# Performance work log

Measured on AMD Instinct MI355X. Metric: run time of the kernel, lower is better.

The kernel has to match this reference:

```python
import jax, jax.numpy as jnp
import numpy as np


def _dct2(x):
    """DCT-II over last dim, scipy norm=None scaling (matches the torch rfft trick:
    X_k = 2 * sum_n x_n cos(pi*k*(2n+1)/(2N))). Expressed as one batched matmul."""
    N = x.shape[-1]
    n = jnp.arange(N, dtype=x.dtype)
    k = jnp.arange(N, dtype=x.dtype)
    # D[k, n] = 2*cos(pi*k*(2n+1)/(2N))
    D = 2.0 * jnp.cos((np.pi / (2.0 * N)) * k[:, None] * (2.0 * n[None, :] + 1.0))
    return jnp.einsum('kn,bcn->bck', D, x)


def setup_inputs() -> dict:
    key = jax.random.key(0)
    k0, k1, k2 = jax.random.split(key, 3)
    b, c, l = 32, 512, 1024
    x = jax.random.normal(k0, (b, c, l), dtype=jnp.float32)
    # 1x1 Conv1d weights (kernel_size=1, bias=False) stored as [out, in]
    w1 = jax.random.normal(k1, (2 * c, c), dtype=jnp.float32) / np.float32(np.sqrt(c))
    w2 = jax.random.normal(k2, (c, 2 * c), dtype=jnp.float32) / np.float32(np.sqrt(2 * c))
    ln_w = jnp.ones((l,), dtype=jnp.float32)
    ln_b = jnp.zeros((l,), dtype=jnp.float32)
    return {"x": x, "w1": w1, "w2": w2, "ln_w": ln_w, "ln_b": ln_b}


def reference(x, w1, w2, ln_w, ln_b):
    eps = 1e-6
    freq = _dct2(x)                                   # [b, c, l]
    mu = jnp.mean(freq, axis=-1, keepdims=True)
    var = jnp.var(freq, axis=-1, keepdims=True)       # biased, like nn.LayerNorm
    h = (freq - mu) * jax.lax.rsqrt(var + eps) * ln_w + ln_b
    # fc: Conv1d(c->2c, k=1) -> Dropout(eval: identity) -> ReLU -> Conv1d(2c->c) -> Sigmoid
    h = jax.nn.relu(jnp.einsum('oi,bil->bol', w1, h))  # [b, 2c, l]
    gate = jax.nn.sigmoid(jnp.einsum('oi,bil->bol', w2, h))  # [b, c, l]
    return x * gate
```

## Files before the change

### kernel.cpp

```cpp
#include <hip/hip_runtime.h>
#include <hip/hip_bf16.h>
#include <math.h>

typedef short short8 __attribute__((ext_vector_type(8)));
typedef short short4v __attribute__((ext_vector_type(4)));
typedef float f32x4 __attribute__((ext_vector_type(4)));

__device__ __forceinline__ short f2bf(float f) {
  union { float f; unsigned u; } v; v.f = f;
  unsigned r = v.u + 0x7FFFu + ((v.u >> 16) & 1u);
  return (short)(r >> 16);
}
__device__ __forceinline__ float bf2f(short s) {
  union { unsigned u; float f; } v; v.u = ((unsigned)(unsigned short)s) << 16;
  return v.f;
}

__global__ __launch_bounds__(256) void cast_kernel(const float* __restrict__ in,
                                                   short* __restrict__ out, int n4) {
  int i = blockIdx.x * blockDim.x + threadIdx.x;
  if (i < n4) {
    float4 v = ((const float4*)in)[i];
    short4v o;
    o.x = f2bf(v.x); o.y = f2bf(v.y); o.z = f2bf(v.z); o.w = f2bf(v.w);
    ((short4v*)out)[i] = o;
  }
}

__global__ __launch_bounds__(256) void prep_eo(const float* __restrict__ x,
                                               short* __restrict__ eo) {
  int t = blockIdx.x * 256 + threadIdx.x;
  int bc = t >> 7, n0 = (t & 127) * 4;
  const float* xr = x + (size_t)bc * 1024;
  float4 f = *(const float4*)(xr + n0);
  float4 r = *(const float4*)(xr + 1020 - n0);
  short4v ef, of;
  ef.x = f2bf(f.x + r.w); ef.y = f2bf(f.y + r.z); ef.z = f2bf(f.z + r.y); ef.w = f2bf(f.w + r.x);
  of.x = f2bf(f.x - r.w); of.y = f2bf(f.y - r.z); of.z = f2bf(f.z - r.y); of.w = f2bf(f.w - r.x);
  *(short4v*)&eo[(size_t)bc * 512 + n0] = ef;
  *(short4v*)&eo[8388608 + (size_t)bc * 512 + n0] = of;
}

__global__ __launch_bounds__(256) void build_Deo(short* __restrict__ D) {
  int t = blockIdx.x * 256 + threadIdx.x;
  int parity = t >> 18, rem = t & 262143;
  int k2 = rem >> 9, n = rem & 511;
  const float s = 1.5339807878856412e-03f;
  float arg = (s * (float)(2 * k2 + parity)) * (float)(2 * n + 1);
  D[t] = f2bf(2.0f * cosf(arg));
}

__global__ __launch_bounds__(256) void ln_stats(const float2* __restrict__ partial,
                                                float2* __restrict__ musd) {
  int n = blockIdx.x * 256 + threadIdx.x;
  float S = 0.f, Q = 0.f;
#pragma unroll
  for (int r = 0; r < 16; ++r) {
    float2 p = partial[(size_t)r * 16384 + n];
    S += p.x; Q += p.y;
  }
  float mu  = S * (1.f / 1024.f);
  float var = Q * (1.f / 1024.f) - mu * mu;
  float2 o; o.x = mu; o.y = rsqrtf(var + 1e-6f);
  musd[n] = o;
}

__global__ __launch_bounds__(256) void ln_apply(short* __restrict__ freqT,
                                                const float2* __restrict__ musd,
                                                const float* __restrict__ lnw,
                                                const float* __restrict__ lnb) {
  int t = blockIdx.x * 256 + threadIdx.x;
  int c8 = t & 63;
  int k  = (t >> 6) & 1023;
  int b  = t >> 16;
  size_t idx = ((size_t)b << 19) + (size_t)k * 512 + (size_t)c8 * 8;
  short8 v = *(const short8*)&freqT[idx];
  float w  = lnw[k];
  float bb = lnb[k];
  const float2* ms = &musd[b * 512 + c8 * 8];
  short8 o;
#pragma unroll
  for (int j = 0; j < 8; ++j) {
    float f = bf2f(v[j]);
    float2 m = ms[j];
    o[j] = f2bf((f - m.x) * m.y * w + bb);
  }
  *(short8*)&freqT[idx] = o;
}

template<int EPI, int MI>
__global__ __launch_bounds__(256, (MI == 2 ? 3 : 2)) void gemmT(
    const short* __restrict__ A, const short* __restrict__ B,
    void* __restrict__ Cout, const float* __restrict__ X,
    float2* __restrict__ P, int K, int NT, long strideA, long strideB)
{
  __shared__ short As[2][MI * 2048];
  __shared__ short Bs[2][8192];
  const int tid = threadIdx.x;
  const int l   = tid & 63;
  const int w   = tid >> 6;
  const int wm  = w >> 1;
  const int wc  = w & 1;
  const int l7  = l & 7;
  const int lr  = l & 15;
  const int lhi = l >> 4;

  const int nwg = gridDim.x, q = nwg >> 3, orig = blockIdx.x;
  const int wgid = (orig & 7) * q + (orig >> 3);
  int bx, by, bz;
  if (EPI == 0)      { bx = wgid & 7; bz = (wgid >> 3) & 1;  by = wgid >> 4; }
  else if (EPI == 1) { by = wgid & 7; bx = (wgid >> 3) & 15; bz = wgid >> 7; }
  else               { bx = wgid & 7; by = (wgid >> 3) & 7;  bz = wgid >> 6; }

  const long row0 = (long)bx * (MI * 32), col0 = (long)by * 128;
  const short* Ab = A + (size_t)bz * strideA + (size_t)row0 * K;
  const short* Bb = B + (size_t)bz * strideB + (size_t)col0 * K;

  const int rowb  = tid >> 3;
  const int slot  = tid & 7;
  const int colel = (slot ^ (rowb & 7)) * 8;
  const int abase = (wm * (MI * 16) + lr) * 64;
  const int bbase = (wc * 64 + lr) * 64;
  const int s0 = ((lhi    ) ^ l7) * 8;
  const int s1 = ((lhi + 4) ^ l7) * 8;

  f32x4 acc[MI][4];
#pragma unroll
  for (int i = 0; i < MI; ++i)
#pragma unroll
    for (int j = 0; j < 4; ++j) acc[i][j] = (f32x4){0.f, 0.f, 0.f, 0.f};

#define GLL(SRC, DST) __builtin_amdgcn_global_load_lds(                      \
      (const __attribute__((address_space(1))) void*)(SRC),                  \
      (__attribute__((address_space(3))) void*)(DST), 16, 0, 0)

#define STAGE(KT, D) do {                                                    \
    const size_t ko_ = (size_t)(KT) * 64 + colel;                            \
    _Pragma("unroll")                                                        \
    for (int r_ = 0; r_ < MI; ++r_)                                          \
      GLL(Ab + (size_t)(r_ * 32 + rowb) * K + ko_,                           \
          &As[D][(r_ * 32 + rowb) * 64 + slot * 8]);                         \
    _Pragma("unroll")                                                        \
    for (int r_ = 0; r_ < 4; ++r_)                                           \
      GLL(Bb + (size_t)(r_ * 32 + rowb) * K + ko_,                           \
          &Bs[D][(r_ * 32 + rowb) * 64 + slot * 8]);                         \
  } while (0)

#define LD8(PTR, OFF) (*(const short8*)&(PTR)[OFF])
#define MFMA(AV, BV, C) __builtin_amdgcn_mfma_f32_16x16x32_bf16(AV, BV, C, 0, 0, 0)
#define SBAR __builtin_amdgcn_s_barrier()
#define SCHB __builtin_amdgcn_sched_barrier(0)

  STAGE(0, 0);
  STAGE(1, 1);

  int cur = 0;
  for (int kt = 0; kt < NT; ++kt) {
    if (kt + 1 < NT) {
      if constexpr (MI == 2) { asm volatile("s_waitcnt vmcnt(6)" ::: "memory"); }
      else                   { asm volatile("s_waitcnt vmcnt(8)" ::: "memory"); }
    } else                   { asm volatile("s_waitcnt vmcnt(0)" ::: "memory"); }
    SCHB; SBAR;
    const short* Ad = As[cur];
    const short* Bd = Bs[cur];
    short8 af0[MI], af1[MI], bf0v[4], bf1v[4];
#pragma unroll
    for (int i = 0; i < MI; ++i) af0[i] = LD8(Ad, abase + i * 1024 + s0);
#pragma unroll
    for (int n = 0; n < 4; ++n)  bf0v[n] = LD8(Bd, bbase + n * 1024 + s0);
#pragma unroll
    for (int i = 0; i < MI; ++i) af1[i] = LD8(Ad, abase + i * 1024 + s1);
#pragma unroll
    for (int n = 0; n < 4; ++n)  bf1v[n] = LD8(Bd, bbase + n * 1024 + s1);
    SCHB;
    if constexpr (MI == 2) { asm volatile("s_waitcnt lgkmcnt(6)" ::: "memory"); }
    else                   { asm volatile("s_waitcnt lgkmcnt(8)" ::: "memory"); }
    SCHB;
    __builtin_amdgcn_s_setprio(1);
#pragma unroll
    for (int i = 0; i < MI; ++i)
#pragma unroll
      for (int n = 0; n < 4; ++n) acc[i][n] = MFMA(af0[i], bf0v[n], acc[i][n]);
    __builtin_amdgcn_s_setprio(0);
    SCHB;
    asm volatile("s_waitcnt lgkmcnt(0)" ::: "memory");
    SCHB; SBAR;
    if (kt + 2 < NT) STAGE(kt + 2, cur);
    SCHB;
    __builtin_amdgcn_s_setprio(1);
#pragma unroll
    for (int i = 0; i < MI; ++i)
#pragma unroll
      for (int n = 0; n < 4; ++n) acc[i][n] = MFMA(af1[i], bf1v[n], acc[i][n]);
    __builtin_amdgcn_s_setprio(0);
    SCHB;
    cur ^= 1;
  }

  float sv[4], qv[4];
#pragma unroll
  for (int ni = 0; ni < 4; ++ni) { sv[ni] = 0.f; qv[ni] = 0.f; }

#pragma unroll
  for (int mi = 0; mi < MI; ++mi) {
#pragma unroll
    for (int ni = 0; ni < 4; ++ni) {
#pragma unroll
      for (int j = 0; j < 4; ++j) {
        int r  = (int)row0 + wm * (MI * 16) + mi * 16 + lhi * 4 + j;
        int cc = (int)col0 + wc * 64 + ni * 16 + lr;
        float v = acc[mi][ni][j];
        if (EPI == 0) {
          sv[ni] += v; qv[ni] += v * v;
          int rr = r * 2 + bz;
          ((short*)Cout)[((size_t)(cc >> 9) << 19) + (size_t)rr * 512 + (cc & 511)] = f2bf(v);
        } else if (EPI == 1) {
          ((short*)Cout)[(size_t)bz * 1048576 + (size_t)r * 1024 + cc] = f2bf(v > 0.f ? v : 0.f);
        } else {
          size_t idx = (size_t)bz * 524288 + (size_t)r * 1024 + cc;
          float g = 1.f / (1.f + __expf(-v));
          ((float*)Cout)[idx] = X[idx] * g;
        }
      }
    }
  }

  if (EPI == 0) {
    __syncthreads();
    float* redS = (float*)&As[0][0];
    float* redQ = redS + 1024;
    const int contrib = wm * 4 + lhi;
#pragma unroll
    for (int ni = 0; ni < 4; ++ni) {
      int ccl = wc * 64 + ni * 16 + lr;
      redS[ccl * 8 + contrib] = sv[ni];
      redQ[ccl * 8 + contrib] = qv[ni];
    }
    __syncthreads();
    if (tid < 128) {
      float S = 0.f, Q = 0.f;
#pragma unroll
      for (int i = 0; i < 8; ++i) { S += redS[tid * 8 + i]; Q += redQ[tid * 8 + i]; }
      float2 o; o.x = S; o.y = Q;
      P[(size_t)(bz * 8 + bx) * 16384 + col0 + tid] = o;
    }
  }
#undef MFMA
#undef LD8
#undef STAGE
#undef GLL
#undef SBAR
#undef SCHB
}

extern "C" void kernel_launch(void* const* d_in, const int* in_sizes, int n_in,
                              void* d_out, int out_size, void* d_ws, size_t ws_size,
                              hipStream_t stream) {
  const float* x    = (const float*)d_in[0];
  const float* w1   = (const float*)d_in[1];
  const float* w2   = (const float*)d_in[2];
  const float* ln_w = (const float*)d_in[3];
  const float* ln_b = (const float*)d_in[4];
  float* out = (float*)d_out;

  char* ws = (char*)d_ws;
  short* Deo    = (short*)(ws);
  short* w1_bf  = (short*)(ws + 1048576);
  short* w2_bf  = (short*)(ws + 2097152);
  short* freqT  = (short*)(ws + 3145728);
  short* z1t    = (short*)(ws + 36700160);
  short* eo     = z1t;
  float2* part  = (float2*)(ws + 103809024);
  float2* musd  = (float2*)(ws + 105906176);

  prep_eo<<<dim3(8192), dim3(256), 0, stream>>>(x, eo);
  cast_kernel<<<dim3(512), dim3(256), 0, stream>>>(w1, w1_bf, 524288 / 4);
  cast_kernel<<<dim3(512), dim3(256), 0, stream>>>(w2, w2_bf, 524288 / 4);
  build_Deo<<<dim3(2048), dim3(256), 0, stream>>>(Deo);

  gemmT<0, 2><<<dim3(2048), dim3(256), 0, stream>>>(
      Deo, eo, (void*)freqT, nullptr, part, 512, 8, 262144, 8388608);

  ln_stats<<<dim3(64), dim3(256), 0, stream>>>(part, musd);

  ln_apply<<<dim3(8192), dim3(256), 0, stream>>>(freqT, musd, ln_w, ln_b);

  gemmT<1, 2><<<dim3(4096), dim3(256), 0, stream>>>(
      freqT, w1_bf, (void*)z1t, nullptr, nullptr, 512, 8, 524288, 0);

  gemmT<2, 2><<<dim3(2048), dim3(256), 0, stream>>>(
      w2_bf, z1t, (void*)out, x, nullptr, 1024, 16, 0, 1048576);
}
```

Baseline: 170.3 us.

## Enlarge GEMM tiles to 256x128 with a K-step of 32

```diff
diff --git a/kernel.cpp b/kernel.cpp
--- a/kernel.cpp
+++ b/kernel.cpp
@@ -55,7 +55,7 @@
   int n = blockIdx.x * 256 + threadIdx.x;
   float S = 0.f, Q = 0.f;
 #pragma unroll
-  for (int r = 0; r < 16; ++r) {
+  for (int r = 0; r < 4; ++r) {
     float2 p = partial[(size_t)r * 16384 + n];
     S += p.x; Q += p.y;
   }
@@ -88,45 +88,40 @@
   *(short8*)&freqT[idx] = o;
 }
 
-template<int EPI, int MI>
-__global__ __launch_bounds__(256, (MI == 2 ? 3 : 2)) void gemmT(
+template<int EPI>
+__global__ __launch_bounds__(256, 2) void gemmF(
     const short* __restrict__ A, const short* __restrict__ B,
     void* __restrict__ Cout, const float* __restrict__ X,
     float2* __restrict__ P, int K, int NT, long strideA, long strideB)
 {
-  __shared__ short As[2][MI * 2048];
-  __shared__ short Bs[2][8192];
+  __shared__ short As[2][8192];
+  __shared__ short Bs[2][4096];
   const int tid = threadIdx.x;
   const int l   = tid & 63;
   const int w   = tid >> 6;
   const int wm  = w >> 1;
   const int wc  = w & 1;
-  const int l7  = l & 7;
   const int lr  = l & 15;
   const int lhi = l >> 4;
 
   const int nwg = gridDim.x, q = nwg >> 3, orig = blockIdx.x;
   const int wgid = (orig & 7) * q + (orig >> 3);
   int bx, by, bz;
-  if (EPI == 0)      { bx = wgid & 7; bz = (wgid >> 3) & 1;  by = wgid >> 4; }
-  else if (EPI == 1) { by = wgid & 7; bx = (wgid >> 3) & 15; bz = wgid >> 7; }
-  else               { bx = wgid & 7; by = (wgid >> 3) & 7;  bz = wgid >> 6; }
-
-  const long row0 = (long)bx * (MI * 32), col0 = (long)by * 128;
+  if (EPI == 0)      { bx = wgid & 1; bz = (wgid >> 1) & 1; by = wgid >> 2; }
+  else if (EPI == 1) { by = wgid & 7; bx = (wgid >> 3) & 3; bz = wgid >> 5; }
+  else               { bx = wgid & 1; by = (wgid >> 1) & 7; bz = wgid >> 4; }
+
+  const long row0 = (long)bx * 256, col0 = (long)by * 128;
   const short* Ab = A + (size_t)bz * strideA + (size_t)row0 * K;
   const short* Bb = B + (size_t)bz * strideB + (size_t)col0 * K;
 
-  const int rowb  = tid >> 3;
-  const int slot  = tid & 7;
-  const int colel = (slot ^ (rowb & 7)) * 8;
-  const int abase = (wm * (MI * 16) + lr) * 64;
-  const int bbase = (wc * 64 + lr) * 64;
-  const int s0 = ((lhi    ) ^ l7) * 8;
-  const int s1 = ((lhi + 4) ^ l7) * 8;
-
-  f32x4 acc[MI][4];
-#pragma unroll
-  for (int i = 0; i < MI; ++i)
+  const int sx    = (lhi ^ ((lr >> 1) & 3)) * 8;
+  const int abase = (wm * 128 + lr) * 32;
+  const int bbase = (wc * 64  + lr) * 32;
+
+  f32x4 acc[8][4];
+#pragma unroll
+  for (int i = 0; i < 8; ++i)
 #pragma unroll
     for (int j = 0; j < 4; ++j) acc[i][j] = (f32x4){0.f, 0.f, 0.f, 0.f};
 
@@ -135,15 +130,19 @@
       (__attribute__((address_space(3))) void*)(DST), 16, 0, 0)
 
 #define STAGE(KT, D) do {                                                    \
-    const size_t ko_ = (size_t)(KT) * 64 + colel;                            \
+    const size_t kb_ = (size_t)(KT) * 32;                                    \
     _Pragma("unroll")                                                        \
-    for (int r_ = 0; r_ < MI; ++r_)                                          \
-      GLL(Ab + (size_t)(r_ * 32 + rowb) * K + ko_,                           \
-          &As[D][(r_ * 32 + rowb) * 64 + slot * 8]);                         \
+    for (int r_ = 0; r_ < 4; ++r_) {                                         \
+      int c_ = r_ * 256 + tid; int row_ = c_ >> 2; int sl_ = c_ & 3;         \
+      int sc_ = (sl_ ^ ((row_ >> 1) & 3)) * 8;                               \
+      GLL(Ab + (size_t)row_ * K + kb_ + sc_, &As[D][row_ * 32 + sl_ * 8]);   \
+    }                                                                        \
     _Pragma("unroll")                                                        \
-    for (int r_ = 0; r_ < 4; ++r_)                                           \
-      GLL(Bb + (size_t)(r_ * 32 + rowb) * K + ko_,                           \
-          &Bs[D][(r_ * 32 + rowb) * 64 + slot * 8]);                         \
+    for (int r_ = 0; r_ < 2; ++r_) {                                         \
+      int c_ = r_ * 256 + tid; int row_ = c_ >> 2; int sl_ = c_ & 3;         \
+      int sc_ = (sl_ ^ ((row_ >> 1) & 3)) * 8;                               \
+      GLL(Bb + (size_t)row_ * K + kb_ + sc_, &Bs[D][row_ * 32 + sl_ * 8]);   \
+    }                                                                        \
   } while (0)
 
 #define LD8(PTR, OFF) (*(const short8*)&(PTR)[OFF])
@@ -151,36 +150,40 @@
 #define SBAR __builtin_amdgcn_s_barrier()
 #define SCHB __builtin_amdgcn_sched_barrier(0)
 
+#define MROW(MI, AV)                                                         \
+    acc[MI][0] = MFMA(AV, b0, acc[MI][0]);                                   \
+    acc[MI][1] = MFMA(AV, b1, acc[MI][1]);                                   \
+    acc[MI][2] = MFMA(AV, b2, acc[MI][2]);                                   \
+    acc[MI][3] = MFMA(AV, b3, acc[MI][3]);
+
   STAGE(0, 0);
   STAGE(1, 1);
 
   int cur = 0;
   for (int kt = 0; kt < NT; ++kt) {
-    if (kt + 1 < NT) {
-      if constexpr (MI == 2) { asm volatile("s_waitcnt vmcnt(6)" ::: "memory"); }
-      else                   { asm volatile("s_waitcnt vmcnt(8)" ::: "memory"); }
-    } else                   { asm volatile("s_waitcnt vmcnt(0)" ::: "memory"); }
+    if (kt + 1 < NT) { asm volatile("s_waitcnt vmcnt(6)" ::: "memory"); }
+    else             { asm volatile("s_waitcnt vmcnt(0)" ::: "memory"); }
     SCHB; SBAR;
     const short* Ad = As[cur];
     const short* Bd = Bs[cur];
-    short8 af0[MI], af1[MI], bf0v[4], bf1v[4];
-#pragma unroll
-    for (int i = 0; i < MI; ++i) af0[i] = LD8(Ad, abase + i * 1024 + s0);
-#pragma unroll
-    for (int n = 0; n < 4; ++n)  bf0v[n] = LD8(Bd, bbase + n * 1024 + s0);
-#pragma unroll
-    for (int i = 0; i < MI; ++i) af1[i] = LD8(Ad, abase + i * 1024 + s1);
-#pragma unroll
-    for (int n = 0; n < 4; ++n)  bf1v[n] = LD8(Bd, bbase + n * 1024 + s1);
-    SCHB;
-    if constexpr (MI == 2) { asm volatile("s_waitcnt lgkmcnt(6)" ::: "memory"); }
-    else                   { asm volatile("s_waitcnt lgkmcnt(8)" ::: "memory"); }
+    short8 a0, a1, a2, a3, a4, a5, a6, a7, b0, b1, b2, b3;
+    a0 = LD8(Ad, abase + 0 * 512 + sx);
+    a1 = LD8(Ad, abase + 1 * 512 + sx);
+    b0 = LD8(Bd, bbase + 0 * 512 + sx);
+    b1 = LD8(Bd, bbase + 1 * 512 + sx);
+    b2 = LD8(Bd, bbase + 2 * 512 + sx);
+    b3 = LD8(Bd, bbase + 3 * 512 + sx);
+    a2 = LD8(Ad, abase + 2 * 512 + sx);
+    a3 = LD8(Ad, abase + 3 * 512 + sx);
+    a4 = LD8(Ad, abase + 4 * 512 + sx);
+    a5 = LD8(Ad, abase + 5 * 512 + sx);
+    a6 = LD8(Ad, abase + 6 * 512 + sx);
+    a7 = LD8(Ad, abase + 7 * 512 + sx);
+    SCHB;
+    asm volatile("s_waitcnt lgkmcnt(6)" ::: "memory");
     SCHB;
     __builtin_amdgcn_s_setprio(1);
-#pragma unroll
-    for (int i = 0; i < MI; ++i)
-#pragma unroll
-      for (int n = 0; n < 4; ++n) acc[i][n] = MFMA(af0[i], bf0v[n], acc[i][n]);
+    MROW(0, a0) MROW(1, a1)
     __builtin_amdgcn_s_setprio(0);
     SCHB;
     asm volatile("s_waitcnt lgkmcnt(0)" ::: "memory");
@@ -188,10 +191,7 @@
     if (kt + 2 < NT) STAGE(kt + 2, cur);
     SCHB;
     __builtin_amdgcn_s_setprio(1);
-#pragma unroll
-    for (int i = 0; i < MI; ++i)
-#pragma unroll
-      for (int n = 0; n < 4; ++n) acc[i][n] = MFMA(af1[i], bf1v[n], acc[i][n]);
+    MROW(2, a2) MROW(3, a3) MROW(4, a4) MROW(5, a5) MROW(6, a6) MROW(7, a7)
     __builtin_amdgcn_s_setprio(0);
     SCHB;
     cur ^= 1;
@@ -202,12 +202,12 @@
   for (int ni = 0; ni < 4; ++ni) { sv[ni] = 0.f; qv[ni] = 0.f; }
 
 #pragma unroll
-  for (int mi = 0; mi < MI; ++mi) {
+  for (int mi = 0; mi < 8; ++mi) {
 #pragma unroll
     for (int ni = 0; ni < 4; ++ni) {
 #pragma unroll
       for (int j = 0; j < 4; ++j) {
-        int r  = (int)row0 + wm * (MI * 16) + mi * 16 + lhi * 4 + j;
+        int r  = (int)row0 + wm * 128 + mi * 16 + lhi * 4 + j;
         int cc = (int)col0 + wc * 64 + ni * 16 + lr;
         float v = acc[mi][ni][j];
         if (EPI == 0) {
@@ -242,9 +242,10 @@
 #pragma unroll
       for (int i = 0; i < 8; ++i) { S += redS[tid * 8 + i]; Q += redQ[tid * 8 + i]; }
       float2 o; o.x = S; o.y = Q;
-      P[(size_t)(bz * 8 + bx) * 16384 + col0 + tid] = o;
+      P[(size_t)(bz * 2 + bx) * 16384 + col0 + tid] = o;
     }
   }
+#undef MROW
 #undef MFMA
 #undef LD8
 #undef STAGE
@@ -271,23 +272,23 @@
   short* z1t    = (short*)(ws + 36700160);
   short* eo     = z1t;
   float2* part  = (float2*)(ws + 103809024);
-  float2* musd  = (float2*)(ws + 105906176);
+  float2* musd  = (float2*)(ws + 104857600);
 
   prep_eo<<<dim3(8192), dim3(256), 0, stream>>>(x, eo);
   cast_kernel<<<dim3(512), dim3(256), 0, stream>>>(w1, w1_bf, 524288 / 4);
   cast_kernel<<<dim3(512), dim3(256), 0, stream>>>(w2, w2_bf, 524288 / 4);
   build_Deo<<<dim3(2048), dim3(256), 0, stream>>>(Deo);
 
-  gemmT<0, 2><<<dim3(2048), dim3(256), 0, stream>>>(
-      Deo, eo, (void*)freqT, nullptr, part, 512, 8, 262144, 8388608);
+  gemmF<0><<<dim3(512), dim3(256), 0, stream>>>(
+      Deo, eo, (void*)freqT, nullptr, part, 512, 16, 262144, 8388608);
 
   ln_stats<<<dim3(64), dim3(256), 0, stream>>>(part, musd);
 
   ln_apply<<<dim3(8192), dim3(256), 0, stream>>>(freqT, musd, ln_w, ln_b);
 
-  gemmT<1, 2><<<dim3(4096), dim3(256), 0, stream>>>(
-      freqT, w1_bf, (void*)z1t, nullptr, nullptr, 512, 8, 524288, 0);
-
-  gemmT<2, 2><<<dim3(2048), dim3(256), 0, stream>>>(
-      w2_bf, z1t, (void*)out, x, nullptr, 1024, 16, 0, 1048576);
-}
+  gemmF<1><<<dim3(1024), dim3(256), 0, stream>>>(
+      freqT, w1_bf, (void*)z1t, nullptr, nullptr, 512, 16, 524288, 0);
+
+  gemmF<2><<<dim3(512), dim3(256), 0, stream>>>(
+      w2_bf, z1t, (void*)out, x, nullptr, 1024, 32, 0, 1048576);
+}
```

New measurement: 159.1 us. 1.07x faster.
